# Kernel optimization log

Hardware: AMD Instinct MI355X
Metric: run time of the kernel (lower is better)

## Reference

```python
import jax, jax.numpy as jnp
import numpy as np
from jax import lax

B, T, N, D = 4, 12, 1024, 128
C_FRONT = 78           # front/back channel split used by the mixup
X_LAST = T // 2 - 1    # static row index of the last (only effective) mixup call
BS_ST = 6              # block_size of mixup_region_ST
SIGMA = 10.0
LN_EPS = 1e-5


def _mixup_region_ST(graph, y):
    """Faithful jax port of mixup_region_ST(graph_front, x=X_LAST, y, 6, sigma=10).
    graph: [T, N, C_FRONT] float; y: traced int scalar."""
    T_, N_, C_ = graph.shape
    x = X_LAST  # static python int
    y_start = jnp.maximum(y - BS_ST, 0)
    y_end = jnp.minimum(y + 2 * BS_ST, N_)

    # temporal gaussian mix of column y over rows [0, x), written at (x, y)
    xs = jnp.arange(x, dtype=graph.dtype)
    w = jnp.exp(-((xs - (x - 1.0)) ** 2) / (2.0 * SIGMA ** 2))
    w = w / w.sum()
    target = graph[:x, y, :]                      # [x, C]
    mixed_value = (w[:, None] * target).sum(0)    # [C]
    g = lax.dynamic_update_slice(graph, mixed_value[None, None, :], (x, y, 0))

    def mix_write(g_, bs, maxj):
        # average blocks g_[:, j*bs:(j+1)*bs, :] for j in [y_start//bs, y_end//bs)
        j0 = y_start // bs
        j1 = y_end // bs
        jj = jnp.arange(maxj)
        mask = (jj < (j1 - j0)).astype(g_.dtype)              # [maxj]
        cols = jnp.clip((j0 + jj)[:, None] * bs + jnp.arange(bs)[None, :], 0, N_ - 1)
        blocks = g_[:, cols, :]                               # [T, maxj, bs, C]
        mixed = (blocks * mask[None, :, None, None]).sum(1) / (j1 - j0).astype(g_.dtype)
        # torch writes mixed_region.to(torch.uint8) into a float tensor
        mixed = lax.stop_gradient(mixed.astype(jnp.uint8).astype(g_.dtype))
        return lax.dynamic_update_slice(g_, mixed, (0, y, 0))

    # torch resets block_size to 1 when y_end > w - block_size
    return lax.cond(y_end > N_ - BS_ST,
                    lambda g_: mix_write(g_, 1, 3 * BS_ST),
                    lambda g_: mix_write(g_, BS_ST, 4),
                    g)


def _forward(inp, adapt_G, xff_w, xff_b, ff1_w, ff1_b, ff2_w, ff2_b, ln_w, ln_b):
    x_ = inp @ xff_w.T + xff_b                       # [B,T,N,3D]
    q, k, v = jnp.split(x_, 3, axis=-1)
    e = jnp.einsum('btnd,btmd->btnm', q, k) / (D ** 0.5)
    e = e @ adapt_G                                  # [B,T,N,N]
    attn = jax.nn.softmax(e, axis=-1)
    attn_det = lax.stop_gradient(attn)               # self.attention_maps = attn.detach()

    def process(attn_b, val_b):                      # [T,N,N], [T,N,D]
        front = val_b[..., :C_FRONT]
        back = val_b[..., C_FRONT:]
        col_sums = attn_b.sum(axis=1)                # [T, N]
        _, idx = lax.top_k(-col_sums, 2)             # 2 smallest per row, ascending
        # only the last loop iteration's mixup survives in the original code
        y = idx[X_LAST, 1]
        return jnp.concatenate([_mixup_region_ST(front, y), back], axis=-1)

    new_value = jax.vmap(process)(attn_det, v)       # [B,T,N,D]
    vi = attn @ new_value                            # [B,T,N,D]
    h = jax.nn.gelu(vi @ ff1_w.T + ff1_b, approximate=False)
    h = h @ ff2_w.T + ff2_b
    out = h + inp
    mu = out.mean(-1, keepdims=True)
    var = ((out - mu) ** 2).mean(-1, keepdims=True)
    return (out - mu) / jnp.sqrt(var + LN_EPS) * ln_w + ln_b


def setup_inputs() -> dict:
    key = jax.random.key(0)
    ks = jax.random.split(key, 6)
    s = 0.02
    return {
        'input': jax.random.normal(ks[0], (B, T, N, D), jnp.float32),
        'adapt_G': jax.random.normal(ks[1], (N, N), jnp.float32) / np.float32(np.sqrt(N)),
        'xff_w': jax.random.normal(ks[2], (3 * D, D), jnp.float32) * s,
        'xff_b': jnp.zeros((3 * D,), jnp.float32),
        'ff1_w': jax.random.normal(ks[3], (D, D), jnp.float32) * s,
        'ff1_b': jnp.zeros((D,), jnp.float32),
        'ff2_w': jax.random.normal(ks[4], (D, D), jnp.float32) * s,
        'ff2_b': jnp.zeros((D,), jnp.float32),
        'ln_w': jnp.ones((D,), jnp.float32),
        'ln_b': jnp.zeros((D,), jnp.float32),
    }


def reference(input, adapt_G, xff_w, xff_b, ff1_w, ff1_b, ff2_w, ff2_b, ln_w, ln_b):
    return _forward(input, adapt_G, xff_w, xff_b, ff1_w, ff1_b, ff2_w, ff2_b, ln_w, ln_b)
```

## Files before the change

kernel.cpp:

```cpp
#include <hip/hip_runtime.h>
#include <hip/hip_bf16.h>

typedef __attribute__((ext_vector_type(8))) short bf16x8;
typedef __attribute__((ext_vector_type(4))) float f32x4;
typedef unsigned long long ull;

#define MFMA(a,b,c) __builtin_amdgcn_mfma_f32_16x16x32_bf16((a),(b),(c),0,0,0)
#define VMCNT(N) asm volatile("s_waitcnt vmcnt(%0)" :: "i"(N) : "memory")
#define EXP2(x) __builtin_amdgcn_exp2f(x)

__device__ __forceinline__ short f2bs(float f){
  union { float f; unsigned u; } x; x.f = f;
  unsigned r = (x.u + 0x7fffu + ((x.u >> 16) & 1u)) >> 16;
  return (short)r;
}
__device__ __forceinline__ float bs2f(short s){
  union { unsigned u; float f; } x; x.u = ((unsigned)(unsigned short)s) << 16;
  return x.f;
}

__device__ __forceinline__ void gl2lds16(const void* g, void* l){
  __builtin_amdgcn_global_load_lds((const __attribute__((address_space(1))) void*)g,
                                   (__attribute__((address_space(3))) void*)l, 16, 0, 0);
}

__device__ __forceinline__ void merge2(ull& a1, ull& a2, ull b1, ull b2){
  ull n1 = min(a1, b1);
  ull n2 = min(max(a1, b1), min(a2, b2));
  a1 = n1; a2 = n2;
}

__global__ __launch_bounds__(256) void prep_kernel(const float* __restrict__ xffw,
                                                   const float* __restrict__ w1,
                                                   const float* __restrict__ w2,
                                                   const float* __restrict__ G,
                                                   short* __restrict__ wqkv_b,
                                                   short* __restrict__ w1_b,
                                                   short* __restrict__ w2_b,
                                                   short* __restrict__ gt){
  __shared__ float tile[32][33];
  int blk = blockIdx.x;
  if (blk >= 1024){
    int i = (blk-1024)*256 + threadIdx.x;
    int stride = 32*256;
    for (int idx = i; idx < 384*128; idx += stride) wqkv_b[idx] = f2bs(xffw[idx]);
    for (int idx = i; idx < 128*128; idx += stride) w1_b[idx] = f2bs(w1[idx]);
    for (int idx = i; idx < 128*128; idx += stride) w2_b[idx] = f2bs(w2[idx]);
    return;
  }
  int bx = blk & 31;
  int by = blk >> 5;
  int tx = threadIdx.x & 31, ty = threadIdx.x >> 5;
  #pragma unroll
  for (int j=0;j<4;j++){
    int n = by*32 + ty + j*8;
    tile[ty+j*8][tx] = G[(size_t)n*1024 + bx*32 + tx];
  }
  __syncthreads();
  #pragma unroll
  for (int j=0;j<4;j++){
    int m = bx*32 + ty + j*8;
    gt[(size_t)m*1024 + by*32 + tx] = f2bs(tile[tx][ty+j*8]);
  }
}

__global__ __launch_bounds__(256,3) void qkv_kernel(const float* __restrict__ inp,
                                                  const short* __restrict__ wqkv,
                                                  const float* __restrict__ bias,
                                                  short* __restrict__ q, short* __restrict__ kT,
                                                  short* __restrict__ nvt){
  __shared__ __align__(16) char smem[49152];
  int w = threadIdx.x >> 6, lane = threadIdx.x & 63;
  int lr = lane & 15, lg = lane >> 4;
  int r0 = blockIdx.x*64;
  int bt = blockIdx.x >> 4;
  int n0 = r0 & 1023;
  int rw = r0 + w*16;
  bf16x8 a[4];
  #pragma unroll
  for (int kc=0;kc<4;kc++){
    const float* ar = inp + (size_t)(rw+lr)*128 + kc*32 + lg*8;
    float4 f0 = *(const float4*)ar;
    float4 f1 = *(const float4*)(ar+4);
    bf16x8 t;
    t[0]=f2bs(f0.x); t[1]=f2bs(f0.y); t[2]=f2bs(f0.z); t[3]=f2bs(f0.w);
    t[4]=f2bs(f1.x); t[5]=f2bs(f1.y); t[6]=f2bs(f1.z); t[7]=f2bs(f1.w);
    a[kc]=t;
  }
  auto stageW = [&](int buf, int kc){
    #pragma unroll
    for (int t=0;t<6;t++){
      int r = (w*6+t)*16 + (lane>>2);
      int s = (lane&3) ^ ((r>>1)&3);
      gl2lds16(wqkv + (size_t)r*128 + kc*32 + s*8,
               smem + buf*24576 + (w*6+t)*1024);
    }
  };
  f32x4 acc[24];
  #pragma unroll
  for (int j=0;j<24;j++) acc[j] = f32x4{0.f,0.f,0.f,0.f};
  stageW(0, 0);
  int cur = 0;
  for (int kc=0; kc<4; kc++){
    if (kc < 3) { stageW(cur^1, kc+1); VMCNT(6); } else { VMCNT(0); }
    __builtin_amdgcn_s_barrier();
    __builtin_amdgcn_sched_barrier(0);
    const char* wb = smem + cur*24576;
    __builtin_amdgcn_s_setprio(1);
    #pragma unroll
    for (int jt=0;jt<24;jt++){
      int j = jt*16 + lr;
      bf16x8 b = *(const bf16x8*)(wb + (size_t)j*64 + ((lg ^ ((lr>>1)&3))*16));
      acc[jt] = MFMA(a[kc], b, acc[jt]);
    }
    __builtin_amdgcn_s_setprio(0);
    __builtin_amdgcn_s_barrier();
    cur ^= 1;
  }
  #pragma unroll
  for (int jt=0;jt<8;jt++){
    float bj = bias[jt*16+lr];
    #pragma unroll
    for (int rr=0;rr<4;rr++)
      q[(size_t)(rw + lg*4 + rr)*128 + jt*16 + lr] = f2bs(acc[jt][rr] + bj);
  }
  __syncthreads();
  short (*tb)[72] = (short(*)[72])smem;
  #pragma unroll
  for (int jt=8;jt<16;jt++){
    int d = (jt-8)*16 + lr;
    float bj = bias[jt*16+lr];
    #pragma unroll
    for (int rr=0;rr<4;rr++) tb[d][w*16 + lg*4 + rr] = f2bs(acc[jt][rr] + bj);
  }
  __syncthreads();
  #pragma unroll
  for (int it=0;it<4;it++){
    int idx = it*256 + threadIdx.x;
    int row = idx >> 3, c8 = (idx & 7)*8;
    *(bf16x8*)(kT + ((size_t)bt*128 + row)*1024 + n0 + c8) = *(const bf16x8*)&tb[row][c8];
  }
  __syncthreads();
  #pragma unroll
  for (int jt=16;jt<24;jt++){
    int c = (jt-16)*16 + lr;
    float bj = bias[jt*16+lr];
    #pragma unroll
    for (int rr=0;rr<4;rr++) tb[c][w*16 + lg*4 + rr] = f2bs(acc[jt][rr] + bj);
  }
  __syncthreads();
  #pragma unroll
  for (int it=0;it<4;it++){
    int idx = it*256 + threadIdx.x;
    int row = idx >> 3, c8 = (idx & 7)*8;
    *(bf16x8*)(nvt + ((size_t)bt*128 + row)*1024 + n0 + c8) = *(const bf16x8*)&tb[row][c8];
  }
}

__global__ __launch_bounds__(256,3) void kg_kernel(const short* __restrict__ gt,
                                                   const short* __restrict__ kT,
                                                   short* __restrict__ kgt){
  __shared__ __align__(16) short gtl[2][64*64];
  __shared__ __align__(16) short ktl[2][128*64];
  int lb = (blockIdx.x & 7)*96 + (blockIdx.x >> 3);
  int bt = lb >> 4;
  int mt = lb & 15;
  int w = threadIdx.x>>6, lane = threadIdx.x&63, lr = lane&15, lg = lane>>4;
  int mblk = mt*64;
  const short* kbase = kT + (size_t)bt*128*1024;
  auto stage = [&](int b, int nc){
    int n0 = nc*64;
    #pragma unroll
    for (int t=0;t<2;t++){
      int row = w*16 + t*8 + (lane>>3);
      int cswz = ((lane&7)*16) ^ ((row&7)<<4);
      gl2lds16(gt + (size_t)(mblk+row)*1024 + n0 + (cswz>>1),
               (char*)gtl[b] + w*2048 + t*1024);
    }
    #pragma unroll
    for (int t=0;t<4;t++){
      int row = w*32 + t*8 + (lane>>3);
      int cswz = ((lane&7)*16) ^ ((row&7)<<4);
      gl2lds16(kbase + (size_t)row*1024 + n0 + (cswz>>1),
               (char*)ktl[b] + w*4096 + t*1024);
    }
  };
  f32x4 acc[8];
  #pragma unroll
  for (int i=0;i<8;i++) acc[i] = f32x4{0.f,0.f,0.f,0.f};
  stage(0, 0);
  int cur = 0;
  for (int nc=0; nc<16; nc++){
    if (nc < 15) { stage(cur^1, nc+1); VMCNT(6); } else { VMCNT(0); }
    __builtin_amdgcn_s_barrier();
    __builtin_amdgcn_sched_barrier(0);
    __builtin_amdgcn_s_setprio(1);
    #pragma unroll
    for (int ks=0;ks<2;ks++){
      int arl = w*16 + lr;
      int acb = ks*64 + lg*16;
      bf16x8 af = *(const bf16x8*)((const char*)gtl[cur] + arl*128 + (acb ^ ((arl&7)<<4)));
      #pragma unroll
      for (int dt=0;dt<8;dt++){
        int brl = dt*16 + lr;
        bf16x8 bf = *(const bf16x8*)((const char*)ktl[cur] + brl*128 + (acb ^ ((brl&7)<<4)));
        acc[dt] = MFMA(af, bf, acc[dt]);
      }
    }
    __builtin_amdgcn_s_setprio(0);
    __builtin_amdgcn_s_barrier();
    cur ^= 1;
  }
  const float SCALE = 0.08838834764831845f * 1.4426950408889634f;
  int m = mblk + w*16 + lg*4;
  #pragma unroll
  for (int dt=0;dt<8;dt++){
    #pragma unroll
    for (int rr=0;rr<4;rr++){
      kgt[((size_t)(bt*1024 + m + rr))*128 + dt*16 + lr] = f2bs(acc[dt][rr]*SCALE);
    }
  }
}

__global__ __launch_bounds__(256,3) void fused_kernel(const short* __restrict__ q,
                                                      const short* __restrict__ kgt,
                                                      const short* __restrict__ nvt,
                                                      float* __restrict__ zbuf,
                                                      short* __restrict__ pbuf,
                                                      short* __restrict__ vib){
  __shared__ __align__(16) short kgl[64*128];
  __shared__ __align__(16) short nvl[128*64];
  __shared__ __align__(16) char  p_raw[8192];
  int lb = (blockIdx.x & 7)*96 + (blockIdx.x >> 3);
  int bt = lb >> 4;
  int rblk = lb & 15;
  int w = threadIdx.x>>6, lane = threadIdx.x&63, lr = lane&15, lg = lane>>4;
  int r0 = rblk*64 + w*16;
  bool is5 = (bt % 12) == 5;
  int bq = bt / 12;
  const short* qrow = q + ((size_t)(bt*1024 + r0 + lr))*128;
  bf16x8 a[4];
  #pragma unroll
  for (int kc=0;kc<4;kc++) a[kc] = *(const bf16x8*)(qrow + kc*32 + lg*8);
  const short* kgb = kgt + (size_t)bt*1024*128;
  const short* nvb = nvt + (size_t)bt*128*1024;
  char* pw = p_raw + w*2048;
  auto stage_kg = [&](int mc){
    int m0 = mc*64;
    #pragma unroll
    for (int t=0;t<4;t++){
      int row = w*16 + t*4 + (lane>>4);
      int cswz = ((lane&15)*16) ^ ((row&7)<<4);
      gl2lds16(kgb + (size_t)(m0+row)*128 + (cswz>>1),
               (char*)kgl + w*4096 + t*1024);
    }
  };
  auto stage_nv = [&](int mc){
    int m0 = mc*64;
    #pragma unroll
    for (int t=0;t<4;t++){
      int row = w*32 + t*8 + (lane>>3);
      int cswz = ((lane&7)*16) ^ ((row&7)<<4);
      gl2lds16(nvb + (size_t)row*1024 + m0 + (cswz>>1),
               (char*)nvl + w*4096 + t*1024);
    }
  };
  f32x4 acc[8];
  #pragma unroll
  for (int i=0;i<8;i++) acc[i] = f32x4{0.f,0.f,0.f,0.f};
  float zacc[4] = {0.f,0.f,0.f,0.f};
  stage_kg(0);
  stage_nv(0);
  VMCNT(0);
  __builtin_amdgcn_s_barrier();
  __builtin_amdgcn_sched_barrier(0);
  for (int mc=0; mc<16; mc++){
    int m0 = mc*64;
    __builtin_amdgcn_s_setprio(1);
    #pragma unroll
    for (int s=0;s<4;s++){
      f32x4 e = f32x4{0.f,0.f,0.f,0.f};
      #pragma unroll
      for (int kc=0;kc<4;kc++){
        int rl = s*16 + lr;
        int cb = kc*64 + lg*16;
        bf16x8 kb = *(const bf16x8*)((const char*)kgl + rl*256 + (cb ^ ((rl&7)<<4)));
        e = MFMA(a[kc], kb, e);
      }
      #pragma unroll
      for (int rr=0;rr<4;rr++){
        int row = lg*4+rr;
        float p = EXP2(fminf(e[rr], 80.f));
        zacc[rr] += p;
        *(short*)(pw + ((row*128 + (s*16+lr)*2) ^ ((row&7)<<4))) = f2bs(p);
      }
    }
    __builtin_amdgcn_s_setprio(0);
    __builtin_amdgcn_s_barrier();
    if (mc < 15) stage_kg(mc+1);
    if (mc < 15) { VMCNT(4); } else { VMCNT(0); }
    __builtin_amdgcn_s_barrier();
    __builtin_amdgcn_sched_barrier(0);
    bf16x8 pa0 = *(const bf16x8*)(pw + ((lr*128 + lg*16) ^ ((lr&7)<<4)));
    bf16x8 pa1 = *(const bf16x8*)(pw + ((lr*128 + 64 + lg*16) ^ ((lr&7)<<4)));
    __builtin_amdgcn_s_setprio(1);
    #pragma unroll
    for (int ct=0; ct<8; ct++){
      int c = ct*16 + lr;
      int mb0 = lg*16;
      int mb1 = 64 + lg*16;
      bf16x8 nb0 = *(const bf16x8*)((const char*)nvl + c*128 + (mb0 ^ ((c&7)<<4)));
      bf16x8 nb1 = *(const bf16x8*)((const char*)nvl + c*128 + (mb1 ^ ((c&7)<<4)));
      acc[ct] = MFMA(pa0, nb0, acc[ct]);
      acc[ct] = MFMA(pa1, nb1, acc[ct]);
    }
    __builtin_amdgcn_s_setprio(0);
    if (is5){
      #pragma unroll
      for (int tt=0; tt<4; tt++){
        int row = tt*4 + (lane>>4);
        int m = (lane&15)*4;
        ull v = *(const ull*)(pw + ((row*128 + m*2) ^ ((row&7)<<4)));
        *(ull*)(pbuf + ((size_t)bq*1024 + r0 + row)*1024 + m0 + m) = v;
      }
    }
    __builtin_amdgcn_s_barrier();
    if (mc < 15) { stage_nv(mc+1); VMCNT(4); } else { VMCNT(0); }
    __builtin_amdgcn_s_barrier();
    __builtin_amdgcn_sched_barrier(0);
  }
  #pragma unroll
  for (int d=1;d<16;d<<=1){
    #pragma unroll
    for (int rr=0;rr<4;rr++) zacc[rr] += __shfl_xor(zacc[rr], d, 64);
  }
  if (lr==0){
    #pragma unroll
    for (int rr=0;rr<4;rr++) zbuf[(size_t)bt*1024 + r0 + lg*4 + rr] = zacc[rr];
  }
  float inv[4];
  #pragma unroll
  for (int rr=0;rr<4;rr++) inv[rr] = 1.0f/zacc[rr];
  #pragma unroll
  for (int ct=0;ct<8;ct++){
    #pragma unroll
    for (int rr=0;rr<4;rr++){
      vib[((size_t)(bt*1024 + r0 + lg*4 + rr))*128 + ct*16 + lr] = f2bs(acc[ct][rr]*inv[rr]);
    }
  }
}

__global__ __launch_bounds__(256) void colsum_kernel(const short* __restrict__ pbuf,
                                                     const float* __restrict__ zbuf,
                                                     float* __restrict__ csfinal){
  __shared__ float part[4][64];
  int b = blockIdx.x >> 4, mg = blockIdx.x & 15;
  int t = threadIdx.x;
  int mcol = mg*64 + (t & 63);
  int rq = t >> 6;
  const short* pb = pbuf + (size_t)b*1024*1024;
  const float* zb = zbuf + (size_t)(b*12 + 5)*1024;
  float s = 0.f;
  for (int r = rq*256; r < rq*256 + 256; r++){
    s += bs2f(pb[(size_t)r*1024 + mcol]) * (1.0f/zb[r]);
  }
  part[rq][t & 63] = s;
  __syncthreads();
  if (t < 64){
    float cs = (part[0][t] + part[1][t]) + (part[2][t] + part[3][t]);
    csfinal[(size_t)b*1024 + mg*64 + t] = cs;
  }
}

__global__ __launch_bounds__(256) void top2_kernel(const float* __restrict__ csfinal,
                                                   int* __restrict__ yidx){
  __shared__ ull s1[4], s2[4];
  int b = blockIdx.x;
  ull b1 = ~0ull, b2 = ~0ull;
  #pragma unroll
  for (int j=0;j<4;j++){
    int col = j*256 + threadIdx.x;
    float s = csfinal[(size_t)b*1024 + col];
    union { float f; unsigned u; } cv; cv.f = s;
    ull key = ((ull)cv.u << 32) | (unsigned)col;
    merge2(b1, b2, key, ~0ull);
  }
  #pragma unroll
  for (int d=1;d<64;d<<=1){
    ull o1 = __shfl_xor(b1, d, 64);
    ull o2 = __shfl_xor(b2, d, 64);
    merge2(b1, b2, o1, o2);
  }
  int w = threadIdx.x >> 6;
  if ((threadIdx.x & 63) == 0){ s1[w] = b1; s2[w] = b2; }
  __syncthreads();
  if (threadIdx.x == 0){
    ull r1 = s1[0], r2 = s2[0];
    merge2(r1, r2, s1[1], s2[1]);
    merge2(r1, r2, s1[2], s2[2]);
    merge2(r1, r2, s1[3], s2[3]);
    yidx[b] = (int)(r2 & 0xffffffffu);
  }
}

__global__ void nvfixA_kernel(const short* __restrict__ nvt, const int* __restrict__ yidx,
                              float* __restrict__ mixres){
  int bt = blockIdx.x; int b = bt/12, t = bt%12;
  int y = yidx[b];
  int y_start = max(y-6, 0), y_end = min(y+12, 1024);
  int bs, j0, cnt;
  if (y_end > 1024-6){ bs = 1; j0 = y_start; cnt = y_end - y_start; }
  else { bs = 6; j0 = y_start/6; cnt = y_end/6 - j0; }
  int items = bs*78;
  int idx = threadIdx.x;
  if (idx >= items) return;
  int i = idx / 78, c = idx % 78;
  const short* nvb = nvt + (size_t)bt*128*1024;
  float acc = 0.f;
  for (int jj=0;jj<cnt;jj++){
    int col = (j0+jj)*bs + i;
    float gv;
    if (t == 5 && col == y){
      float wsum = 0.f, mv = 0.f;
      #pragma unroll
      for (int tp=0;tp<5;tp++){
        float d = (float)tp - 4.0f;
        float w = __expf(-d*d/200.0f);
        wsum += w;
        mv += w * bs2f(nvt[((size_t)(b*12+tp)*128 + c)*1024 + y]);
      }
      gv = mv / wsum;
    } else {
      gv = bs2f(nvb[(size_t)c*1024 + col]);
    }
    acc += gv;
  }
  mixres[((size_t)bt*6 + i)*78 + c] = acc / (float)cnt;
}

__global__ __launch_bounds__(256,3) void ffn_kernel(const short* __restrict__ vib,
                                                  const float* __restrict__ inp,
                                                  const short* __restrict__ w1b,
                                                  const short* __restrict__ w2b,
                                                  const float* __restrict__ b1,
                                                  const float* __restrict__ b2,
                                                  const float* __restrict__ lnw,
                                                  const float* __restrict__ lnb,
                                                  const short* __restrict__ qb,
                                                  const short* __restrict__ kgt,
                                                  const short* __restrict__ nvt,
                                                  const float* __restrict__ mixres,
                                                  const float* __restrict__ zbuf,
                                                  const int* __restrict__ yidx,
                                                  float* __restrict__ out){
  __shared__ __align__(16) short wl[128*128];
  __shared__ __align__(16) char  hb[4*16*132*2];
  short* kcolT = (short*)hb;
  float* delta = (float*)(hb + 4352);
  float* p_sh  = (float*)(hb + 4352 + 1920);
  short* hs    = (short*)hb;
  int w = threadIdx.x>>6, lane = threadIdx.x&63, lr = lane&15, lg = lane>>4;
  int bt = blockIdx.x >> 4;
  int nb = (blockIdx.x & 15)*64;
  int r0 = blockIdx.x*64 + w*16;
  int b = bt/12;
  int y = yidx[b];
  int y_end = min(y+12, 1024);
  int bs = (y_end > 1024-6) ? 1 : 6;
  for (int idx = threadIdx.x; idx < 16*128; idx += 256){
    int i = idx >> 7, d = idx & 127;
    kcolT[i*136 + d] = (i < bs) ? kgt[((size_t)(bt*1024 + y + i))*128 + d] : (short)0;
  }
  for (int idx = threadIdx.x; idx < 6*78; idx += 256){
    int i = idx / 78, c = idx % 78;
    float dv = 0.f;
    if (i < bs){
      float avg = mixres[((size_t)bt*6 + i)*78 + c];
      int ti = (int)avg;
      unsigned char u = (unsigned char)ti;
      dv = (float)u - bs2f(nvt[((size_t)bt*128 + c)*1024 + (y+i)]);
    }
    delta[i*80 + c] = dv;
  }
  __syncthreads();
  {
    const short* qr = qb + ((size_t)(bt*1024 + nb + w*16 + lr))*128;
    bf16x8 qa[4];
    #pragma unroll
    for (int kc=0;kc<4;kc++) qa[kc] = *(const bf16x8*)(qr + kc*32 + lg*8);
    f32x4 ep = f32x4{0.f,0.f,0.f,0.f};
    #pragma unroll
    for (int kc=0;kc<4;kc++){
      bf16x8 kb = *(const bf16x8*)((const char*)kcolT + lr*272 + kc*64 + lg*16);
      ep = MFMA(qa[kc], kb, ep);
    }
    #pragma unroll
    for (int rr=0;rr<4;rr++){
      int row = w*16 + lg*4 + rr;
      float pv = 0.f;
      if (lr < bs){
        float z = zbuf[(size_t)bt*1024 + nb + row];
        pv = EXP2(fminf(ep[rr], 80.f)) / z;
      }
      if (lr < 6) p_sh[row*6 + lr] = pv;
    }
  }
  auto stageW = [&](const short* src){
    #pragma unroll
    for (int t=0;t<8;t++){
      int r = (w*8+t)*4 + (lane>>4);
      int s = (lane&15) ^ (r&7);
      gl2lds16(src + (size_t)r*128 + s*8, (char*)wl + (w*8+t)*1024);
    }
  };
  stageW(w1b);
  __syncthreads();
  float pr6[6];
  #pragma unroll
  for (int i=0;i<6;i++) pr6[i] = p_sh[(w*16 + lr)*6 + i];
  bf16x8 a[4];
  #pragma unroll
  for (int kc=0;kc<4;kc++){
    bf16x8 v = *(const bf16x8*)(vib + (size_t)(r0+lr)*128 + kc*32 + lg*8);
    #pragma unroll
    for (int e=0;e<8;e++){
      int col = kc*32 + lg*8 + e;
      if (col < 78){
        float ds = 0.f;
        #pragma unroll
        for (int i=0;i<6;i++) ds += pr6[i] * delta[i*80 + col];
        v[e] = f2bs(bs2f(v[e]) + ds);
      }
    }
    a[kc] = v;
  }
  __syncthreads();
  f32x4 acc[8];
  #pragma unroll
  for (int i=0;i<8;i++) acc[i] = f32x4{0.f,0.f,0.f,0.f};
  __builtin_amdgcn_s_setprio(1);
  #pragma unroll
  for (int kc=0;kc<4;kc++){
    #pragma unroll
    for (int jt=0;jt<8;jt++){
      bf16x8 bfr = *(const bf16x8*)((const char*)wl + (size_t)(jt*16+lr)*256 + (((kc*4+lg) ^ (lr&7))*16));
      acc[jt] = MFMA(a[kc], bfr, acc[jt]);
    }
  }
  __builtin_amdgcn_s_setprio(0);
  #pragma unroll
  for (int jt=0;jt<8;jt++){
    float bj = b1[jt*16+lr];
    #pragma unroll
    for (int rr=0;rr<4;rr++){
      float x = acc[jt][rr] + bj;
      float g = 0.5f*x*(1.0f + erff(x*0.70710678118654752f));
      hs[(w*16 + lg*4 + rr)*132 + jt*16 + lr] = f2bs(g);
    }
  }
  __syncthreads();
  stageW(w2b);
  bf16x8 ha[4];
  #pragma unroll
  for (int kc=0;kc<4;kc++){
    const short* hp = &hs[(w*16 + lr)*132 + kc*32 + lg*8];
    ull lo = *(const ull*)hp;
    ull hi = *(const ull*)(hp + 4);
    ((ull*)&ha[kc])[0] = lo; ((ull*)&ha[kc])[1] = hi;
  }
  __syncthreads();
  f32x4 acc2[8];
  #pragma unroll
  for (int i=0;i<8;i++) acc2[i] = f32x4{0.f,0.f,0.f,0.f};
  __builtin_amdgcn_s_setprio(1);
  #pragma unroll
  for (int kc=0;kc<4;kc++){
    #pragma unroll
    for (int jt=0;jt<8;jt++){
      bf16x8 bfr = *(const bf16x8*)((const char*)wl + (size_t)(jt*16+lr)*256 + (((kc*4+lg) ^ (lr&7))*16));
      acc2[jt] = MFMA(ha[kc], bfr, acc2[jt]);
    }
  }
  __builtin_amdgcn_s_setprio(0);
  float xv[8][4];
  #pragma unroll
  for (int jt=0;jt<8;jt++){
    float bj = b2[jt*16+lr];
    #pragma unroll
    for (int rr=0;rr<4;rr++){
      xv[jt][rr] = acc2[jt][rr] + bj + inp[(size_t)(r0 + lg*4 + rr)*128 + jt*16 + lr];
    }
  }
  float mu[4], rstd[4];
  #pragma unroll
  for (int rr=0;rr<4;rr++){
    float s = 0.f;
    #pragma unroll
    for (int jt=0;jt<8;jt++) s += xv[jt][rr];
    #pragma unroll
    for (int m=1;m<16;m<<=1) s += __shfl_xor(s, m, 64);
    mu[rr] = s * (1.0f/128.0f);
  }
  #pragma unroll
  for (int rr=0;rr<4;rr++){
    float s = 0.f;
    #pragma unroll
    for (int jt=0;jt<8;jt++){ float d = xv[jt][rr]-mu[rr]; s += d*d; }
    #pragma unroll
    for (int m=1;m<16;m<<=1) s += __shfl_xor(s, m, 64);
    rstd[rr] = rsqrtf(s * (1.0f/128.0f) + 1e-5f);
  }
  #pragma unroll
  for (int jt=0;jt<8;jt++){
    int col = jt*16 + lr;
    float lw = lnw[col], lb = lnb[col];
    #pragma unroll
    for (int rr=0;rr<4;rr++){
      out[(size_t)(r0 + lg*4 + rr)*128 + col] = (xv[jt][rr]-mu[rr])*rstd[rr]*lw + lb;
    }
  }
}

extern "C" void kernel_launch(void* const* d_in, const int* in_sizes, int n_in,
                              void* d_out, int out_size, void* d_ws, size_t ws_size,
                              hipStream_t stream) {
  (void)in_sizes; (void)n_in; (void)out_size;
  const float* inp  = (const float*)d_in[0];
  const float* G    = (const float*)d_in[1];
  const float* xffw = (const float*)d_in[2];
  const float* xffb = (const float*)d_in[3];
  const float* w1   = (const float*)d_in[4];
  const float* b1   = (const float*)d_in[5];
  const float* w2   = (const float*)d_in[6];
  const float* b2   = (const float*)d_in[7];
  const float* lnw  = (const float*)d_in[8];
  const float* lnb  = (const float*)d_in[9];
  float* out = (float*)d_out;
  char* ws = (char*)d_ws;

  size_t off = 0;
  auto take = [&](size_t bytes)->char*{ char* p = ws + off; off += (bytes + 255) & ~(size_t)255; return p; };
  short* wqkv_b = (short*)take(384*128*2);
  short* gt_b   = (short*)take((size_t)1024*1024*2);
  short* w1_b   = (short*)take(128*128*2);
  short* w2_b   = (short*)take(128*128*2);
  short* qb     = (short*)take((size_t)48*1024*128*2);
  short* kTb    = (short*)take((size_t)48*128*1024*2);
  short* nvt    = (short*)take((size_t)48*128*1024*2);
  short* kgt    = (short*)take((size_t)48*1024*128*2);
  float* zbuf   = (float*)take((size_t)48*1024*4);
  short* pbuf   = (short*)take((size_t)4*1024*1024*2);
  float* csfin  = (float*)take((size_t)4*1024*4);
  int*   yidx   = (int*)take(256);
  float* mixres = (float*)take((size_t)48*6*78*4);
  short* vibuf  = (short*)take((size_t)48*1024*128*2);
  if (off > ws_size) return;

  prep_kernel<<<dim3(1056), dim3(256), 0, stream>>>(xffw, w1, w2, G, wqkv_b, w1_b, w2_b, gt_b);
  qkv_kernel<<<dim3(768), dim3(256), 0, stream>>>(inp, wqkv_b, xffb, qb, kTb, nvt);
  kg_kernel<<<dim3(768), dim3(256), 0, stream>>>(gt_b, kTb, kgt);
  fused_kernel<<<dim3(768), dim3(256), 0, stream>>>(qb, kgt, nvt, zbuf, pbuf, vibuf);
  colsum_kernel<<<dim3(64), dim3(256), 0, stream>>>(pbuf, zbuf, csfin);
  top2_kernel<<<dim3(4), dim3(256), 0, stream>>>(csfin, yidx);
  nvfixA_kernel<<<dim3(48), dim3(512), 0, stream>>>(nvt, yidx, mixres);
  ffn_kernel<<<dim3(768), dim3(256), 0, stream>>>(vibuf, inp, w1_b, w2_b, b1, b2, lnw, lnb,
                                                  qb, kgt, nvt, mixres, zbuf, yidx, out);
}
```

Before: 136.2 us.

## Stage FFN weights in K-halves to halve LDS and raise occupancy

The FFN kernel now stages each 128x128 bf16 weight matrix into LDS as two 64-column halves rather than all at once. This halves the weight buffer and raises the launch-bounds occupancy target from 3 to 4 blocks per CU. It also issues the first W1 half-stage and the vib loads earlier, and prefetches the residual input into registers while the second W2 half loads. The cost is extra barriers and a second staging round per GEMM. The added register arrays (rin, av) may cause spills under the tighter register budget.

```diff
diff --git a/kernel.cpp b/kernel.cpp
--- a/kernel.cpp
+++ b/kernel.cpp
@@ -438,7 +438,7 @@
   mixres[((size_t)bt*6 + i)*78 + c] = acc / (float)cnt;
 }
 
-__global__ __launch_bounds__(256,3) void ffn_kernel(const short* __restrict__ vib,
+__global__ __launch_bounds__(256,4) void ffn_kernel(const short* __restrict__ vib,
                                                   const float* __restrict__ inp,
                                                   const short* __restrict__ w1b,
                                                   const short* __restrict__ w2b,
@@ -453,8 +453,8 @@
                                                   const float* __restrict__ zbuf,
                                                   const int* __restrict__ yidx,
                                                   float* __restrict__ out){
-  __shared__ __align__(16) short wl[128*128];
-  __shared__ __align__(16) char  hb[4*16*132*2];
+  __shared__ __align__(16) short wl[128*64];
+  __shared__ __align__(16) char  hb[16896];
   short* kcolT = (short*)hb;
   float* delta = (float*)(hb + 4352);
   float* p_sh  = (float*)(hb + 4352 + 1920);
@@ -467,6 +467,18 @@
   int y = yidx[b];
   int y_end = min(y+12, 1024);
   int bs = (y_end > 1024-6) ? 1 : 6;
+  auto stageH = [&](const short* src, int half){
+    #pragma unroll
+    for (int t=0;t<4;t++){
+      int r = (w*4+t)*8 + (lane>>3);
+      int s = (lane&7) ^ (r&7);
+      gl2lds16(src + (size_t)r*128 + half*64 + s*8, (char*)wl + (w*4+t)*1024);
+    }
+  };
+  stageH(w1b, 0);
+  bf16x8 av[4];
+  #pragma unroll
+  for (int kc=0;kc<4;kc++) av[kc] = *(const bf16x8*)(vib + (size_t)(r0+lr)*128 + kc*32 + lg*8);
   for (int idx = threadIdx.x; idx < 16*128; idx += 256){
     int i = idx >> 7, d = idx & 127;
     kcolT[i*136 + d] = (i < bs) ? kgt[((size_t)(bt*1024 + y + i))*128 + d] : (short)0;
@@ -505,15 +517,6 @@
       if (lr < 6) p_sh[row*6 + lr] = pv;
     }
   }
-  auto stageW = [&](const short* src){
-    #pragma unroll
-    for (int t=0;t<8;t++){
-      int r = (w*8+t)*4 + (lane>>4);
-      int s = (lane&15) ^ (r&7);
-      gl2lds16(src + (size_t)r*128 + s*8, (char*)wl + (w*8+t)*1024);
-    }
-  };
-  stageW(w1b);
   __syncthreads();
   float pr6[6];
   #pragma unroll
@@ -521,7 +524,7 @@
   bf16x8 a[4];
   #pragma unroll
   for (int kc=0;kc<4;kc++){
-    bf16x8 v = *(const bf16x8*)(vib + (size_t)(r0+lr)*128 + kc*32 + lg*8);
+    bf16x8 v = av[kc];
     #pragma unroll
     for (int e=0;e<8;e++){
       int col = kc*32 + lg*8 + e;
@@ -534,16 +537,30 @@
     }
     a[kc] = v;
   }
-  __syncthreads();
   f32x4 acc[8];
   #pragma unroll
   for (int i=0;i<8;i++) acc[i] = f32x4{0.f,0.f,0.f,0.f};
   __builtin_amdgcn_s_setprio(1);
   #pragma unroll
-  for (int kc=0;kc<4;kc++){
+  for (int kc=0;kc<2;kc++){
     #pragma unroll
     for (int jt=0;jt<8;jt++){
-      bf16x8 bfr = *(const bf16x8*)((const char*)wl + (size_t)(jt*16+lr)*256 + (((kc*4+lg) ^ (lr&7))*16));
+      int jr = jt*16 + lr;
+      bf16x8 bfr = *(const bf16x8*)((const char*)wl + (size_t)jr*128 + (((kc*4+lg) ^ (jr&7))*16));
+      acc[jt] = MFMA(a[kc], bfr, acc[jt]);
+    }
+  }
+  __builtin_amdgcn_s_setprio(0);
+  __syncthreads();
+  stageH(w1b, 1);
+  __syncthreads();
+  __builtin_amdgcn_s_setprio(1);
+  #pragma unroll
+  for (int kc=2;kc<4;kc++){
+    #pragma unroll
+    for (int jt=0;jt<8;jt++){
+      int jr = jt*16 + lr;
+      bf16x8 bfr = *(const bf16x8*)((const char*)wl + (size_t)jr*128 + ((((kc-2)*4+lg) ^ (jr&7))*16));
       acc[jt] = MFMA(a[kc], bfr, acc[jt]);
     }
   }
@@ -559,7 +576,7 @@
     }
   }
   __syncthreads();
-  stageW(w2b);
+  stageH(w2b, 0);
   bf16x8 ha[4];
   #pragma unroll
   for (int kc=0;kc<4;kc++){
@@ -574,10 +591,31 @@
   for (int i=0;i<8;i++) acc2[i] = f32x4{0.f,0.f,0.f,0.f};
   __builtin_amdgcn_s_setprio(1);
   #pragma unroll
-  for (int kc=0;kc<4;kc++){
+  for (int kc=0;kc<2;kc++){
     #pragma unroll
     for (int jt=0;jt<8;jt++){
-      bf16x8 bfr = *(const bf16x8*)((const char*)wl + (size_t)(jt*16+lr)*256 + (((kc*4+lg) ^ (lr&7))*16));
+      int jr = jt*16 + lr;
+      bf16x8 bfr = *(const bf16x8*)((const char*)wl + (size_t)jr*128 + (((kc*4+lg) ^ (jr&7))*16));
+      acc2[jt] = MFMA(ha[kc], bfr, acc2[jt]);
+    }
+  }
+  __builtin_amdgcn_s_setprio(0);
+  __syncthreads();
+  stageH(w2b, 1);
+  float rin[8][4];
+  #pragma unroll
+  for (int jt=0;jt<8;jt++)
+    #pragma unroll
+    for (int rr=0;rr<4;rr++)
+      rin[jt][rr] = inp[(size_t)(r0 + lg*4 + rr)*128 + jt*16 + lr];
+  __syncthreads();
+  __builtin_amdgcn_s_setprio(1);
+  #pragma unroll
+  for (int kc=2;kc<4;kc++){
+    #pragma unroll
+    for (int jt=0;jt<8;jt++){
+      int jr = jt*16 + lr;
+      bf16x8 bfr = *(const bf16x8*)((const char*)wl + (size_t)jr*128 + ((((kc-2)*4+lg) ^ (jr&7))*16));
       acc2[jt] = MFMA(ha[kc], bfr, acc2[jt]);
     }
   }
@@ -588,7 +626,7 @@
     float bj = b2[jt*16+lr];
     #pragma unroll
     for (int rr=0;rr<4;rr++){
-      xv[jt][rr] = acc2[jt][rr] + bj + inp[(size_t)(r0 + lg*4 + rr)*128 + jt*16 + lr];
+      xv[jt][rr] = acc2[jt][rr] + bj + rin[jt][rr];
     }
   }
   float mu[4], rstd[4];
```

Result: slower. 141.7 us (+4.0%).
